# Kernel optimization log

Hardware: AMD Instinct MI355X
Metric: run time of the kernel (lower is better)

Reference implementation:

```python
import jax, jax.numpy as jnp
import numpy as np

H = 64  # GRU hidden size (hard-coded in module)


def _gru_scan(x_proj, w_hh, b_hh):
    """Run a single-direction GRU (torch gate order r,z,n).

    x_proj: [T, B, 3H] precomputed input projections (x @ W_ih^T + b_ih)
    w_hh:   [3H, H], b_hh: [3H]
    Returns all hidden states [T, B, H].
    """
    w_hr, w_hz, w_hn = w_hh[:H], w_hh[H:2 * H], w_hh[2 * H:]
    b_hr, b_hz, b_hn = b_hh[:H], b_hh[H:2 * H], b_hh[2 * H:]
    B = x_proj.shape[1]
    h0 = jnp.zeros((B, H), dtype=x_proj.dtype)

    def step(h, xp):
        xr, xz, xn = xp[:, :H], xp[:, H:2 * H], xp[:, 2 * H:]
        r = jax.nn.sigmoid(xr + h @ w_hr.T + b_hr)
        z = jax.nn.sigmoid(xz + h @ w_hz.T + b_hz)
        n = jnp.tanh(xn + r * (h @ w_hn.T + b_hn))
        h_new = (1.0 - z) * n + z * h
        return h_new, h_new

    _, hs = jax.lax.scan(step, h0, x_proj)
    return hs  # [T, B, H]


def setup_inputs() -> dict:
    key = jax.random.key(0)
    ks = jax.random.split(key, 11)
    B, T, D = 512, 512, 32
    s_ih = 1.0 / np.sqrt(H)
    u = lambda k, shape: jax.random.uniform(k, shape, jnp.float32, -s_ih, s_ih)
    return {
        "x": jax.random.normal(ks[0], (B, T, D), dtype=jnp.float32),
        # forward direction GRU params
        "w_ih_f": u(ks[1], (3 * H, D)),
        "w_hh_f": u(ks[2], (3 * H, H)),
        "b_ih_f": u(ks[3], (3 * H,)),
        "b_hh_f": u(ks[4], (3 * H,)),
        # backward direction GRU params
        "w_ih_b": u(ks[5], (3 * H, D)),
        "w_hh_b": u(ks[6], (3 * H, H)),
        "b_ih_b": u(ks[7], (3 * H,)),
        "b_hh_b": u(ks[8], (3 * H,)),
        # fc head: Linear(128,64) -> LeakyReLU(0.2) -> Linear(64,1)
        "fc1_w": jax.random.normal(ks[9], (64, 2 * H), dtype=jnp.float32) * (1.0 / np.sqrt(2 * H)),
        "fc1_b": jnp.zeros((64,), dtype=jnp.float32),
        "fc2_w": jax.random.normal(ks[10], (1, 64), dtype=jnp.float32) * (1.0 / np.sqrt(64)),
        "fc2_b": jnp.zeros((1,), dtype=jnp.float32),
    }


def reference(x, w_ih_f, w_hh_f, b_ih_f, b_hh_f,
              w_ih_b, w_hh_b, b_ih_b, b_hh_b,
              fc1_w, fc1_b, fc2_w, fc2_b):
    # x: [B, T, D] -> time-major [T, B, D]
    xt = jnp.swapaxes(x, 0, 1)
    # precompute input projections for all timesteps (one big GEMM per dir)
    xp_f = jnp.einsum('tbd,gd->tbg', xt, w_ih_f) + b_ih_f  # [T,B,3H]
    xp_b = jnp.einsum('tbd,gd->tbg', xt, w_ih_b) + b_ih_b

    hs_f = _gru_scan(xp_f, w_hh_f, b_hh_f)            # forward over t=0..T-1
    hs_b = _gru_scan(xp_b[::-1], w_hh_b, b_hh_b)      # backward: reversed time
    # out[:, -1, :] = concat(fwd hidden at t=T-1, bwd hidden at t=T-1).
    # bwd hidden at original t=T-1 is the FIRST step of the reversed scan.
    last = jnp.concatenate([hs_f[-1], hs_b[0]], axis=-1)  # [B, 2H]

    h1 = last @ fc1_w.T + fc1_b
    h1 = jnp.where(h1 >= 0, h1, 0.2 * h1)  # LeakyReLU(0.2)
    return h1 @ fc2_w.T + fc2_b  # [B, 1]
```

## Files before the change

### kernel.cpp

```cpp
#include <hip/hip_runtime.h>

namespace {
constexpr int T = 512;
constexpr int BATCH = 512;
constexpr int D = 32;
constexpr int H = 64;
constexpr int THREADS = 128;
}

typedef float v2f __attribute__((ext_vector_type(2)));

__device__ __forceinline__ float rcpf(float x) { return __builtin_amdgcn_rcpf(x); }
__device__ __forceinline__ float sigm(float x) { return rcpf(1.0f + __expf(-x)); }
__device__ __forceinline__ float tanh_fast(float x) {
    return 1.0f - 2.0f * rcpf(__expf(2.0f * x) + 1.0f);
}

__device__ __forceinline__ void pk2(v2f& acc, v2f w, v2f v) {
    asm("v_pk_fma_f32 %0, %1, %2, %0" : "+v"(acc) : "v"(w), "v"(v));
}

__device__ __forceinline__ float pair_sum(float v) {
    int i = __builtin_bit_cast(int, v);
    float t = __builtin_bit_cast(float,
        __builtin_amdgcn_update_dpp(0, i, 0xB1, 0xF, 0xF, true));
    return v + t;
}

__global__ __launch_bounds__(THREADS, 1) void gru_fused_kernel(
    const float* __restrict__ x,
    const float* __restrict__ w_ih_f, const float* __restrict__ w_hh_f,
    const float* __restrict__ b_ih_f, const float* __restrict__ b_hh_f,
    const float* __restrict__ w_ih_b, const float* __restrict__ b_ih_b,
    const float* __restrict__ b_hh_b,
    const float* __restrict__ fc1_w, const float* __restrict__ fc1_b,
    const float* __restrict__ fc2_w, const float* __restrict__ fc2_b,
    float* __restrict__ out)
{
    const int b   = blockIdx.x;
    const int tid = threadIdx.x;
    const int j   = tid >> 1;
    const int q   = tid & 1;
    const int kh0 = q * 32;
    const int kx0 = q * 16;

    __shared__ v2f x_lds[T * D / 2];
    __shared__ __align__(16) float h_lds[2][H];
    __shared__ float last_lds[2 * H];

    v2f wr2[16], wz2[16], wn2[16], ur2[8], uz2[8], un2[8];
    {
        const v2f* pr = reinterpret_cast<const v2f*>(w_hh_f + (size_t)j * H + kh0);
        const v2f* pz = reinterpret_cast<const v2f*>(w_hh_f + (size_t)(H + j) * H + kh0);
        const v2f* pn = reinterpret_cast<const v2f*>(w_hh_f + (size_t)(2 * H + j) * H + kh0);
        #pragma unroll
        for (int m = 0; m < 16; ++m) { wr2[m] = pr[m]; wz2[m] = pz[m]; wn2[m] = pn[m]; }
        const v2f* qr = reinterpret_cast<const v2f*>(w_ih_f + (size_t)j * D + kx0);
        const v2f* qz = reinterpret_cast<const v2f*>(w_ih_f + (size_t)(H + j) * D + kx0);
        const v2f* qn = reinterpret_cast<const v2f*>(w_ih_f + (size_t)(2 * H + j) * D + kx0);
        #pragma unroll
        for (int m = 0; m < 8; ++m) { ur2[m] = qr[m]; uz2[m] = qz[m]; un2[m] = qn[m]; }
    }

    const float pre_r  = b_ih_f[j]         + b_hh_f[j];
    const float pre_z  = b_ih_f[H + j]     + b_hh_f[H + j];
    const float pre_nx = b_ih_f[2 * H + j];
    const float pre_nh = b_hh_f[2 * H + j];

    {
        const float4* xg  = reinterpret_cast<const float4*>(x + (size_t)b * T * D);
        float4*       xl4 = reinterpret_cast<float4*>(x_lds);
        #pragma unroll 4
        for (int i = tid; i < T * D / 4; i += THREADS) xl4[i] = xg[i];
    }
    if (tid < H) h_lds[0][tid] = 0.0f;
    __syncthreads();

    v2f axr = {0.f, 0.f}, axz = {0.f, 0.f}, axn = {0.f, 0.f};
    {
        const v2f* xt2 = x_lds + q * 8;
        #pragma unroll
        for (int m = 0; m < 8; ++m) {
            v2f xv = xt2[m];
            pk2(axr, ur2[m], xv);
            pk2(axz, uz2[m], xv);
            pk2(axn, un2[m], xv);
        }
    }

    float hold = 0.0f;

    for (int t = 0; t < T; ++t) {
        const int cur = t & 1, nxt = cur ^ 1;

        v2f hh[16];
        {
            const v2f* hp = reinterpret_cast<const v2f*>(&h_lds[cur][kh0]);
            #pragma unroll
            for (int m = 0; m < 16; ++m) hh[m] = hp[m];
        }

        v2f pr = axr, pz = axz, nh = {0.f, 0.f};
        #pragma unroll
        for (int m = 0; m < 16; ++m) pk2(pr, wr2[m], hh[m]);
        #pragma unroll
        for (int m = 0; m < 16; ++m) pk2(pz, wz2[m], hh[m]);
        #pragma unroll
        for (int m = 0; m < 16; ++m) pk2(nh, wn2[m], hh[m]);
        const v2f axn_t = axn;

        {
            const int tn = (t + 1) & (T - 1);
            const v2f* xt2 = x_lds + tn * (D / 2) + q * 8;
            axr = {0.f, 0.f}; axz = {0.f, 0.f}; axn = {0.f, 0.f};
            #pragma unroll
            for (int m = 0; m < 8; ++m) {
                v2f xv = xt2[m];
                pk2(axr, ur2[m], xv);
                pk2(axz, uz2[m], xv);
                pk2(axn, un2[m], xv);
            }
        }

        const float vr  = pair_sum(pr.x + pr.y);
        const float vz  = pair_sum(pz.x + pz.y);
        const float vnh = pair_sum(nh.x + nh.y);
        const float vnx = pair_sum(axn_t.x + axn_t.y);

        const float r = sigm(vr + pre_r);
        const float z = sigm(vz + pre_z);
        const float n = tanh_fast(vnx + pre_nx + r * (vnh + pre_nh));
        const float hnew = n + z * (hold - n);
        hold = hnew;
        if (q == 0) h_lds[nxt][j] = hnew;
        __syncthreads();
    }

    const int wave = tid >> 6, lane = tid & 63;

    if (wave == 0) last_lds[lane] = h_lds[T & 1][lane];

    if (wave == 1) {
        const float* xT = reinterpret_cast<const float*>(x_lds) + (T - 1) * D;
        const int jj = lane;
        float xr = b_ih_b[jj];
        float xz = b_ih_b[H + jj];
        float xn = b_ih_b[2 * H + jj];
        #pragma unroll
        for (int k = 0; k < D; ++k) {
            const float xv = xT[k];
            xr = fmaf(w_ih_b[(size_t)jj * D + k],           xv, xr);
            xz = fmaf(w_ih_b[(size_t)(H + jj) * D + k],     xv, xz);
            xn = fmaf(w_ih_b[(size_t)(2 * H + jj) * D + k], xv, xn);
        }
        const float r = sigm(xr + b_hh_b[jj]);
        const float z = sigm(xz + b_hh_b[H + jj]);
        const float n = tanh_fast(xn + r * b_hh_b[2 * H + jj]);
        last_lds[H + jj] = (1.0f - z) * n;
    }
    __syncthreads();

    if (wave == 0) {
        float acc = fc1_b[lane];
        const float* w1 = fc1_w + (size_t)lane * (2 * H);
        #pragma unroll 8
        for (int c = 0; c < 2 * H; ++c) acc = fmaf(w1[c], last_lds[c], acc);
        acc = (acc >= 0.0f) ? acc : 0.2f * acc;
        float red = acc * fc2_w[lane];
        #pragma unroll
        for (int off = 32; off > 0; off >>= 1)
            red += __shfl_down(red, off);
        if (lane == 0) out[b] = red + fc2_b[0];
    }
}

extern "C" void kernel_launch(void* const* d_in, const int* in_sizes, int n_in,
                              void* d_out, int out_size, void* d_ws, size_t ws_size,
                              hipStream_t stream) {
    const float* x      = (const float*)d_in[0];
    const float* w_ih_f = (const float*)d_in[1];
    const float* w_hh_f = (const float*)d_in[2];
    const float* b_ih_f = (const float*)d_in[3];
    const float* b_hh_f = (const float*)d_in[4];
    const float* w_ih_b = (const float*)d_in[5];
    const float* b_ih_b = (const float*)d_in[7];
    const float* b_hh_b = (const float*)d_in[8];
    const float* fc1_w  = (const float*)d_in[9];
    const float* fc1_b  = (const float*)d_in[10];
    const float* fc2_w  = (const float*)d_in[11];
    const float* fc2_b  = (const float*)d_in[12];
    float* out = (float*)d_out;

    gru_fused_kernel<<<BATCH, THREADS, 0, stream>>>(
        x, w_ih_f, w_hh_f, b_ih_f, b_hh_f,
        w_ih_b, b_ih_b, b_hh_b,
        fc1_w, fc1_b, fc2_w, fc2_b, out);
}
```

Before: 203.4 us.

## Process two batch rows per block with interleaved GRU recurrences

Each block now runs the forward GRU recurrence for two batch rows at once, so the grid shrinks to half as many blocks. The register-resident recurrent weights are reused for both chains, and the two independent dependency chains are interleaved for more instruction-level parallelism. One barrier per timestep now serves both rows. Only row A's inputs are staged in LDS; row B's inputs are read from global memory two steps ahead. The trade-offs are fewer waves per CU, more register pressure, and global-load latency on the recurrent critical path.

After: 370.5 us. 82.2% more time.

```diff
diff --git a/kernel.cpp b/kernel.cpp
--- a/kernel.cpp
+++ b/kernel.cpp
@@ -6,9 +6,11 @@
 constexpr int D = 32;
 constexpr int H = 64;
 constexpr int THREADS = 128;
+constexpr int ROWS = 2;
 }
 
 typedef float v2f __attribute__((ext_vector_type(2)));
+typedef float v4f __attribute__((ext_vector_type(4)));
 
 __device__ __forceinline__ float rcpf(float x) { return __builtin_amdgcn_rcpf(x); }
 __device__ __forceinline__ float sigm(float x) { return rcpf(1.0f + __expf(-x)); }
@@ -37,16 +39,18 @@
     const float* __restrict__ fc2_w, const float* __restrict__ fc2_b,
     float* __restrict__ out)
 {
-    const int b   = blockIdx.x;
     const int tid = threadIdx.x;
     const int j   = tid >> 1;
     const int q   = tid & 1;
     const int kh0 = q * 32;
     const int kx0 = q * 16;
 
-    __shared__ v2f x_lds[T * D / 2];
-    __shared__ __align__(16) float h_lds[2][H];
-    __shared__ float last_lds[2 * H];
+    const int rowA = blockIdx.x * ROWS;
+    const int rowB = rowA + 1;
+
+    __shared__ v4f x_lds[T * D / 4];
+    __shared__ __align__(16) float h_lds[ROWS][2][H];
+    __shared__ float last_lds[ROWS][2 * H];
 
     v2f wr2[16], wz2[16], wn2[16], ur2[8], uz2[8], un2[8];
     {
@@ -67,110 +71,160 @@
     const float pre_nx = b_ih_f[2 * H + j];
     const float pre_nh = b_hh_f[2 * H + j];
 
-    {
-        const float4* xg  = reinterpret_cast<const float4*>(x + (size_t)b * T * D);
-        float4*       xl4 = reinterpret_cast<float4*>(x_lds);
+    const float* xrowA = x + (size_t)rowA * T * D;
+    const float* xrowB = x + (size_t)rowB * T * D;
+
+    {
+        const v4f* xg = reinterpret_cast<const v4f*>(xrowA);
         #pragma unroll 4
-        for (int i = tid; i < T * D / 4; i += THREADS) xl4[i] = xg[i];
-    }
-    if (tid < H) h_lds[0][tid] = 0.0f;
+        for (int i = tid; i < T * D / 4; i += THREADS) x_lds[i] = xg[i];
+    }
+    if (tid < H) { h_lds[0][0][tid] = 0.0f; h_lds[1][0][tid] = 0.0f; }
     __syncthreads();
 
-    v2f axr = {0.f, 0.f}, axz = {0.f, 0.f}, axn = {0.f, 0.f};
-    {
-        const v2f* xt2 = x_lds + q * 8;
+    v2f axrA = {0.f,0.f}, axzA = {0.f,0.f}, axnA = {0.f,0.f};
+    {
+        const v2f* xt2 = reinterpret_cast<const v2f*>(x_lds) + q * 8;
         #pragma unroll
         for (int m = 0; m < 8; ++m) {
             v2f xv = xt2[m];
-            pk2(axr, ur2[m], xv);
-            pk2(axz, uz2[m], xv);
-            pk2(axn, un2[m], xv);
-        }
-    }
-
-    float hold = 0.0f;
+            pk2(axrA, ur2[m], xv); pk2(axzA, uz2[m], xv); pk2(axnA, un2[m], xv);
+        }
+    }
+    v2f axrB = {0.f,0.f}, axzB = {0.f,0.f}, axnB = {0.f,0.f};
+    {
+        const v2f* px = reinterpret_cast<const v2f*>(xrowB + kx0);
+        #pragma unroll
+        for (int m = 0; m < 8; ++m) {
+            v2f xv = px[m];
+            pk2(axrB, ur2[m], xv); pk2(axzB, uz2[m], xv); pk2(axnB, un2[m], xv);
+        }
+    }
+    v4f nxB[4];
+    {
+        const v4f* px = reinterpret_cast<const v4f*>(xrowB + D + kx0);
+        nxB[0] = px[0]; nxB[1] = px[1]; nxB[2] = px[2]; nxB[3] = px[3];
+    }
+
+    float holdA = 0.0f, holdB = 0.0f;
 
     for (int t = 0; t < T; ++t) {
         const int cur = t & 1, nxt = cur ^ 1;
 
-        v2f hh[16];
-        {
-            const v2f* hp = reinterpret_cast<const v2f*>(&h_lds[cur][kh0]);
-            #pragma unroll
-            for (int m = 0; m < 16; ++m) hh[m] = hp[m];
-        }
-
-        v2f pr = axr, pz = axz, nh = {0.f, 0.f};
-        #pragma unroll
-        for (int m = 0; m < 16; ++m) pk2(pr, wr2[m], hh[m]);
-        #pragma unroll
-        for (int m = 0; m < 16; ++m) pk2(pz, wz2[m], hh[m]);
-        #pragma unroll
-        for (int m = 0; m < 16; ++m) pk2(nh, wn2[m], hh[m]);
-        const v2f axn_t = axn;
+        v2f hhA[16];
+        {
+            const v2f* hp = reinterpret_cast<const v2f*>(&h_lds[0][cur][kh0]);
+            #pragma unroll
+            for (int m = 0; m < 16; ++m) hhA[m] = hp[m];
+        }
+        v2f prA = axrA, pzA = axzA, nhA = {0.f,0.f};
+        #pragma unroll
+        for (int m = 0; m < 16; ++m) pk2(prA, wr2[m], hhA[m]);
+        #pragma unroll
+        for (int m = 0; m < 16; ++m) pk2(pzA, wz2[m], hhA[m]);
+        #pragma unroll
+        for (int m = 0; m < 16; ++m) pk2(nhA, wn2[m], hhA[m]);
+        const v2f axnA_t = axnA;
+
+        v2f hhB[16];
+        {
+            const v2f* hp = reinterpret_cast<const v2f*>(&h_lds[1][cur][kh0]);
+            #pragma unroll
+            for (int m = 0; m < 16; ++m) hhB[m] = hp[m];
+        }
+        v2f prB = axrB, pzB = axzB, nhB = {0.f,0.f};
+        #pragma unroll
+        for (int m = 0; m < 16; ++m) pk2(prB, wr2[m], hhB[m]);
+        #pragma unroll
+        for (int m = 0; m < 16; ++m) pk2(pzB, wz2[m], hhB[m]);
+        #pragma unroll
+        for (int m = 0; m < 16; ++m) pk2(nhB, wn2[m], hhB[m]);
+        const v2f axnB_t = axnB;
 
         {
             const int tn = (t + 1) & (T - 1);
-            const v2f* xt2 = x_lds + tn * (D / 2) + q * 8;
-            axr = {0.f, 0.f}; axz = {0.f, 0.f}; axn = {0.f, 0.f};
+            const v2f* xt2 = reinterpret_cast<const v2f*>(x_lds) + tn * (D / 2) + q * 8;
+            axrA = {0.f,0.f}; axzA = {0.f,0.f}; axnA = {0.f,0.f};
             #pragma unroll
             for (int m = 0; m < 8; ++m) {
                 v2f xv = xt2[m];
-                pk2(axr, ur2[m], xv);
-                pk2(axz, uz2[m], xv);
-                pk2(axn, un2[m], xv);
+                pk2(axrA, ur2[m], xv); pk2(axzA, uz2[m], xv); pk2(axnA, un2[m], xv);
             }
         }
 
-        const float vr  = pair_sum(pr.x + pr.y);
-        const float vz  = pair_sum(pz.x + pz.y);
-        const float vnh = pair_sum(nh.x + nh.y);
-        const float vnx = pair_sum(axn_t.x + axn_t.y);
-
-        const float r = sigm(vr + pre_r);
-        const float z = sigm(vz + pre_z);
-        const float n = tanh_fast(vnx + pre_nx + r * (vnh + pre_nh));
-        const float hnew = n + z * (hold - n);
-        hold = hnew;
-        if (q == 0) h_lds[nxt][j] = hnew;
+        {
+            axrB = {0.f,0.f}; axzB = {0.f,0.f}; axnB = {0.f,0.f};
+            #pragma unroll
+            for (int mm = 0; mm < 4; ++mm) {
+                v2f lo = __builtin_shufflevector(nxB[mm], nxB[mm], 0, 1);
+                v2f hi = __builtin_shufflevector(nxB[mm], nxB[mm], 2, 3);
+                pk2(axrB, ur2[2*mm], lo); pk2(axrB, ur2[2*mm+1], hi);
+                pk2(axzB, uz2[2*mm], lo); pk2(axzB, uz2[2*mm+1], hi);
+                pk2(axnB, un2[2*mm], lo); pk2(axnB, un2[2*mm+1], hi);
+            }
+        }
+
+        {
+            const v4f* px = reinterpret_cast<const v4f*>(
+                xrowB + ((t + 2) & (T - 1)) * D + kx0);
+            nxB[0] = px[0]; nxB[1] = px[1]; nxB[2] = px[2]; nxB[3] = px[3];
+        }
+
+        const float vrA  = pair_sum(prA.x + prA.y);
+        const float vzA  = pair_sum(pzA.x + pzA.y);
+        const float vnhA = pair_sum(nhA.x + nhA.y);
+        const float vnxA = pair_sum(axnA_t.x + axnA_t.y);
+        const float vrB  = pair_sum(prB.x + prB.y);
+        const float vzB  = pair_sum(pzB.x + pzB.y);
+        const float vnhB = pair_sum(nhB.x + nhB.y);
+        const float vnxB = pair_sum(axnB_t.x + axnB_t.y);
+
+        const float rA = sigm(vrA + pre_r);
+        const float zA = sigm(vzA + pre_z);
+        const float rB = sigm(vrB + pre_r);
+        const float zB = sigm(vzB + pre_z);
+        const float nA = tanh_fast(vnxA + pre_nx + rA * (vnhA + pre_nh));
+        const float nB = tanh_fast(vnxB + pre_nx + rB * (vnhB + pre_nh));
+        const float hnewA = nA + zA * (holdA - nA);
+        const float hnewB = nB + zB * (holdB - nB);
+        holdA = hnewA; holdB = hnewB;
+        if (q == 0) { h_lds[0][nxt][j] = hnewA; h_lds[1][nxt][j] = hnewB; }
         __syncthreads();
     }
 
     const int wave = tid >> 6, lane = tid & 63;
-
-    if (wave == 0) last_lds[lane] = h_lds[T & 1][lane];
-
-    if (wave == 1) {
-        const float* xT = reinterpret_cast<const float*>(x_lds) + (T - 1) * D;
-        const int jj = lane;
-        float xr = b_ih_b[jj];
-        float xz = b_ih_b[H + jj];
-        float xn = b_ih_b[2 * H + jj];
+    const float* xrow_w = (wave == 0) ? xrowA : xrowB;
+
+    {
+        const float* xT = xrow_w + (size_t)(T - 1) * D;
+        float xr = b_ih_b[lane];
+        float xz = b_ih_b[H + lane];
+        float xn = b_ih_b[2 * H + lane];
         #pragma unroll
         for (int k = 0; k < D; ++k) {
             const float xv = xT[k];
-            xr = fmaf(w_ih_b[(size_t)jj * D + k],           xv, xr);
-            xz = fmaf(w_ih_b[(size_t)(H + jj) * D + k],     xv, xz);
-            xn = fmaf(w_ih_b[(size_t)(2 * H + jj) * D + k], xv, xn);
-        }
-        const float r = sigm(xr + b_hh_b[jj]);
-        const float z = sigm(xz + b_hh_b[H + jj]);
-        const float n = tanh_fast(xn + r * b_hh_b[2 * H + jj]);
-        last_lds[H + jj] = (1.0f - z) * n;
-    }
-    __syncthreads();
-
-    if (wave == 0) {
+            xr = fmaf(w_ih_b[(size_t)lane * D + k],           xv, xr);
+            xz = fmaf(w_ih_b[(size_t)(H + lane) * D + k],     xv, xz);
+            xn = fmaf(w_ih_b[(size_t)(2 * H + lane) * D + k], xv, xn);
+        }
+        const float r = sigm(xr + b_hh_b[lane]);
+        const float z = sigm(xz + b_hh_b[H + lane]);
+        const float n = tanh_fast(xn + r * b_hh_b[2 * H + lane]);
+        last_lds[wave][H + lane] = (1.0f - z) * n;
+    }
+    last_lds[wave][lane] = h_lds[wave][0][lane];
+
+    {
         float acc = fc1_b[lane];
         const float* w1 = fc1_w + (size_t)lane * (2 * H);
         #pragma unroll 8
-        for (int c = 0; c < 2 * H; ++c) acc = fmaf(w1[c], last_lds[c], acc);
+        for (int c = 0; c < 2 * H; ++c) acc = fmaf(w1[c], last_lds[wave][c], acc);
         acc = (acc >= 0.0f) ? acc : 0.2f * acc;
         float red = acc * fc2_w[lane];
         #pragma unroll
         for (int off = 32; off > 0; off >>= 1)
             red += __shfl_down(red, off);
-        if (lane == 0) out[b] = red + fc2_b[0];
+        if (lane == 0) out[rowA + wave] = red + fc2_b[0];
     }
 }
 
@@ -191,7 +245,7 @@
     const float* fc2_b  = (const float*)d_in[12];
     float* out = (float*)d_out;
 
-    gru_fused_kernel<<<BATCH, THREADS, 0, stream>>>(
+    gru_fused_kernel<<<BATCH / ROWS, THREADS, 0, stream>>>(
         x, w_ih_f, w_hh_f, b_ih_f, b_hh_f,
         w_ih_b, b_ih_b, b_hh_b,
         fc1_w, fc1_b, fc2_w, fc2_b, out);
```
